# Kernel tuning notes

Measured on AMD Instinct MI355X. Metric: run time of the kernel, lower is better.

Reference implementation:

```python
import jax, jax.numpy as jnp
import numpy as np

N, E, D_IN, D_HID, D_OUT, G = 50000, 800000, 64, 64, 64, 64
BN_EPS = 1e-5


def gcn_conv(x, W, b, src, dst, n_nodes):
    """PyG GCNConv: add self-loops, sym-normalized sum aggregation, then bias.
    out_i = sum_{j->i} d_j^-1/2 d_i^-1/2 (x W)_j + d_i^-1 (x W)_i + b
    where d_i = 1 + in-degree(i) (self-loop included)."""
    h = x @ W  # [N, out]
    deg = jax.ops.segment_sum(jnp.ones((src.shape[0],), h.dtype), dst,
                              num_segments=n_nodes) + 1.0  # self-loop
    dinv = jax.lax.rsqrt(deg)  # deg >= 1 always
    coef = dinv[src] * dinv[dst]  # [E]
    msgs = h[src] * coef[:, None]  # [E, out] -- the big gather
    agg = jax.ops.segment_sum(msgs, dst, num_segments=n_nodes)
    agg = agg + h * (dinv * dinv)[:, None]  # self-loop messages
    return agg + b


def global_mean_pool(x, batch, n_graphs):
    sums = jax.ops.segment_sum(x, batch, num_segments=n_graphs)
    cnts = jax.ops.segment_sum(jnp.ones((x.shape[0],), x.dtype), batch,
                               num_segments=n_graphs)
    return sums / jnp.maximum(cnts, 1.0)[:, None]


def setup_inputs() -> dict:
    key = jax.random.key(0)
    ks = jax.random.split(key, 8)
    x = jax.random.normal(ks[0], (N, D_IN), dtype=jnp.float32)
    edge_index = jax.random.randint(ks[1], (2, E), 0, N, dtype=jnp.int32)
    batch = jnp.sort(jax.random.randint(ks[2], (N,), 0, G, dtype=jnp.int32))
    s1 = 1.0 / np.sqrt(D_IN)
    s2 = 1.0 / np.sqrt(D_HID)
    W1 = jax.random.uniform(ks[3], (D_IN, D_HID), jnp.float32, -s1, s1)
    b1 = jnp.zeros((D_HID,), jnp.float32)
    gamma = jnp.ones((D_HID,), jnp.float32)
    beta = jnp.zeros((D_HID,), jnp.float32)
    W2 = jax.random.uniform(ks[4], (D_HID, D_OUT), jnp.float32, -s2, s2)
    b2 = jnp.zeros((D_OUT,), jnp.float32)
    return {"x": x, "edge_index": edge_index, "batch": batch,
            "W1": W1, "b1": b1, "gamma": gamma, "beta": beta,
            "W2": W2, "b2": b2}


def reference(x, edge_index, batch, W1, b1, gamma, beta, W2, b2):
    src, dst = edge_index[0], edge_index[1]
    h = gcn_conv(x, W1, b1, src, dst, N)
    # BatchNorm1d with batch statistics (training-mode forward)
    mu = jnp.mean(h, axis=0)
    var = jnp.mean(jnp.square(h - mu), axis=0)
    h = (h - mu) * jax.lax.rsqrt(var + BN_EPS) * gamma + beta
    h = jax.nn.elu(h)
    # dropout is identity in eval / deterministic reference
    out = gcn_conv(h, W2, b2, src, dst, N)
    graph_rep = global_mean_pool(out, batch, G)
    return (out, graph_rep)
```

## Files before the change

kernel.cpp:

```cpp
#include <hip/hip_runtime.h>


constexpr int GGRAPHS = 64;
constexpr int EPB = 4096;
constexpr int CNTB = 128;

__global__ void fat_phist_cnt_mm64_kernel(
    const int* __restrict__ dst, const int* __restrict__ batch,
    int* __restrict__ hist, int* __restrict__ cnt,
    const float* __restrict__ X, const float* __restrict__ W,
    float* __restrict__ Y,
    int E, int n, int nblk, int nbuck) {
  __shared__ float Ws[64][64];
  __shared__ float xs[4][64];
  __shared__ int h[256];
  __shared__ int hb[GGRAPHS];
  int t = threadIdx.x;
  int bid = blockIdx.x;
  if (bid < nblk) {
    h[t] = 0;
    __syncthreads();
    int e0 = bid * EPB;
    int e1 = e0 + EPB < E ? e0 + EPB : E;
    for (int i = e0 + t; i < e1; i += 256) {
      int d = dst[i];
      if ((unsigned)d < (unsigned)n) atomicAdd(&h[d >> 8], 1);
    }
    __syncthreads();
    if (t < nbuck) hist[t * nblk + bid] = h[t];
  } else if (bid < nblk + CNTB) {
    int cb = bid - nblk;
    if (t < GGRAPHS) hb[t] = 0;
    __syncthreads();
    for (int i = cb * 256 + t; i < n; i += CNTB * 256) {
      int g = batch[i];
      if ((unsigned)g < (unsigned)GGRAPHS) atomicAdd(&hb[g], 1);
    }
    __syncthreads();
    if (t < GGRAPHS && hb[t] > 0) atomicAdd(&cnt[t], hb[t]);
  } else {
    int mb = bid - nblk - CNTB;
    for (int i = t; i < 64 * 64; i += 256) Ws[i >> 6][i & 63] = W[i];
    int rr = t >> 6, c = t & 63;
    int row = mb * 4 + rr;
    xs[rr][c] = (row < n) ? X[(size_t)row * 64 + c] : 0.0f;
    __syncthreads();
    float acc = 0.0f;
#pragma unroll
    for (int k = 0; k < 64; ++k) acc = fmaf(xs[rr][k], Ws[k][c], acc);
    if (row < n) Y[(size_t)row * 64 + c] = acc;
  }
}

__global__ void scan1_kernel(const int* __restrict__ in, int* __restrict__ out,
                             int* __restrict__ bsum, int n) {
  __shared__ int tmp[256];
  int t = threadIdx.x;
  int i = blockIdx.x * 256 + t;
  int v = (i < n) ? in[i] : 0;
  tmp[t] = v;
  __syncthreads();
#pragma unroll
  for (int off = 1; off < 256; off <<= 1) {
    int a = (t >= off) ? tmp[t - off] : 0;
    __syncthreads();
    tmp[t] += a;
    __syncthreads();
  }
  if (i < n) out[i] = tmp[t] - v;
  if (t == 255) bsum[blockIdx.x] = tmp[255];
}

__global__ void scan_add2_kernel(int* __restrict__ data, const int* __restrict__ bsum,
                                 int S, int nbt) {
  __shared__ int tmp[256];
  int t = threadIdx.x;
  int v = (t < nbt) ? bsum[t] : 0;
  tmp[t] = v;
  __syncthreads();
#pragma unroll
  for (int off = 1; off < 256; off <<= 1) {
    int a = (t >= off) ? tmp[t - off] : 0;
    __syncthreads();
    tmp[t] += a;
    __syncthreads();
  }
  int pre = (blockIdx.x == 0) ? 0 : tmp[blockIdx.x - 1];
  int i = blockIdx.x * 256 + t;
  if (i < S) data[i] += pre;
  if (i == 0) data[S] = tmp[nbt - 1];
}

__global__ void part_kernel(const int* __restrict__ srcp, const int* __restrict__ dstp,
                            const int* __restrict__ hist, int* __restrict__ part,
                            int E, int n, int nblk, int nbuck) {
  __shared__ int cur[256];
  int t = threadIdx.x;
  if (t < nbuck) cur[t] = hist[t * nblk + blockIdx.x];
  __syncthreads();
  int e0 = blockIdx.x * EPB;
  int e1 = e0 + EPB < E ? e0 + EPB : E;
  for (int i = e0 + t; i < e1; i += 256) {
    int d = dstp[i];
    if ((unsigned)d >= (unsigned)n) continue;
    int s = srcp[i];
    int pos = atomicAdd(&cur[d >> 8], 1);
    part[pos] = (s << 8) | (d & 255);
  }
}

__global__ void csr_kernel(const int* __restrict__ part, const int* __restrict__ hist,
                           int* __restrict__ rowptr, float* __restrict__ dinv,
                           int* __restrict__ col, int n, int nblk, int nbuck) {
  __shared__ int degL[256], scn[256], cur[256];
  int t = threadIdx.x;
  int b = blockIdx.x;
  degL[t] = 0;
  cur[t] = 0;
  __syncthreads();
  int base = hist[b * nblk];
  int end = hist[(b + 1) * nblk];
  for (int i = base + t; i < end; i += 256) atomicAdd(&degL[part[i] & 255], 1);
  __syncthreads();
  int dv = degL[t];
  scn[t] = dv;
  __syncthreads();
#pragma unroll
  for (int off = 1; off < 256; off <<= 1) {
    int a = (t >= off) ? scn[t - off] : 0;
    __syncthreads();
    scn[t] += a;
    __syncthreads();
  }
  int excl = scn[t] - dv;
  int node = (b << 8) + t;
  if (node < n) {
    rowptr[node] = base + excl;
    dinv[node] = rsqrtf((float)dv + 1.0f);
  }
  if (b == nbuck - 1 && t == 0) rowptr[n] = end;
  scn[t] = excl;
  __syncthreads();
  for (int i = base + t; i < end; i += 256) {
    int u = part[i];
    int d = u & 255;
    int k = atomicAdd(&cur[d], 1);
    col[base + scn[d] + k] = u >> 8;
  }
}

__global__ void bn_elu_mm64_kernel(const float* __restrict__ X, const float* __restrict__ W,
                                   const float* __restrict__ ss, float* __restrict__ Y, int n) {
  __shared__ float Ws[64][64];
  __shared__ float xs[4][64];
  int tid = threadIdx.x;
  for (int i = tid; i < 64 * 64; i += 256) Ws[i >> 6][i & 63] = W[i];
  int rr = tid >> 6, c = tid & 63;
  int row = blockIdx.x * 4 + rr;
  float v = 0.0f;
  if (row < n) {
    v = X[(size_t)row * 64 + c] * ss[c] + ss[64 + c];
    v = v > 0.0f ? v : expm1f(v);
  }
  xs[rr][c] = v;
  __syncthreads();
  float acc = 0.0f;
#pragma unroll
  for (int k = 0; k < 64; ++k) acc = fmaf(xs[rr][k], Ws[k][c], acc);
  if (row < n) Y[(size_t)row * 64 + c] = acc;
}

__device__ __forceinline__ float4 gcn_gather_core(
    const int* __restrict__ rowptr, const int* __restrict__ col,
    const float* __restrict__ dinv, const float4* __restrict__ H4,
    int row, int lane, int sub, int cg, bool valid) {
  float4 acc = make_float4(0.f, 0.f, 0.f, 0.f);
  int p0 = 0, p1 = 0;
  if (valid) { p0 = rowptr[row]; p1 = rowptr[row + 1]; }
  for (int base = p0; base < p1; base += 64) {
    int myp = base + lane;
    int j = (myp < p1) ? col[myp] : 0;
    float w = (myp < p1) ? dinv[j] : 0.0f;
    int m = p1 - base;
    m = m < 64 ? m : 64;
#pragma unroll 4
    for (int k = 0; k < m; k += 4) {
      int s = k + sub;
      int jj = __shfl(j, s);
      float ww = __shfl(w, s);
      float4 hv = H4[(size_t)jj * 16 + cg];
      acc.x = fmaf(hv.x, ww, acc.x);
      acc.y = fmaf(hv.y, ww, acc.y);
      acc.z = fmaf(hv.z, ww, acc.z);
      acc.w = fmaf(hv.w, ww, acc.w);
    }
  }
  acc.x += __shfl_xor(acc.x, 16);
  acc.y += __shfl_xor(acc.y, 16);
  acc.z += __shfl_xor(acc.z, 16);
  acc.w += __shfl_xor(acc.w, 16);
  acc.x += __shfl_xor(acc.x, 32);
  acc.y += __shfl_xor(acc.y, 32);
  acc.z += __shfl_xor(acc.z, 32);
  acc.w += __shfl_xor(acc.w, 32);
  return acc;
}

__global__ void gather_bn_kernel(const int* __restrict__ rowptr, const int* __restrict__ col,
                                 const float* __restrict__ dinv, const float* __restrict__ H,
                                 const float* __restrict__ b, float* __restrict__ OUT,
                                 float* __restrict__ bnsR, int n) {
  int wave = threadIdx.x >> 6;
  int lane = threadIdx.x & 63;
  int row = blockIdx.x * 4 + wave;
  bool valid = row < n;
  int sub = lane >> 4;
  int cg = lane & 15;
  const float4* __restrict__ H4 = (const float4*)H;
  float4 acc = gcn_gather_core(rowptr, col, dinv, H4, row, lane, sub, cg, valid);
  float4 o = make_float4(0.f, 0.f, 0.f, 0.f);
  if (valid) {
    float di = dinv[row];
    float d2 = di * di;
    float4 self = H4[(size_t)row * 16 + cg];
    float4 bb = ((const float4*)b)[cg];
    o.x = fmaf(acc.x, di, fmaf(self.x, d2, bb.x));
    o.y = fmaf(acc.y, di, fmaf(self.y, d2, bb.y));
    o.z = fmaf(acc.z, di, fmaf(self.z, d2, bb.z));
    o.w = fmaf(acc.w, di, fmaf(self.w, d2, bb.w));
    if (sub == 0) ((float4*)OUT)[(size_t)row * 16 + cg] = o;
  }
  __shared__ float sA[4][64], sB[4][64];
  if (sub == 0) {
    sA[wave][4 * cg + 0] = o.x;
    sA[wave][4 * cg + 1] = o.y;
    sA[wave][4 * cg + 2] = o.z;
    sA[wave][4 * cg + 3] = o.w;
    sB[wave][4 * cg + 0] = o.x * o.x;
    sB[wave][4 * cg + 1] = o.y * o.y;
    sB[wave][4 * cg + 2] = o.z * o.z;
    sB[wave][4 * cg + 3] = o.w * o.w;
  }
  __syncthreads();
  int t = threadIdx.x;
  if (t < 64) {
    float s = sA[0][t] + sA[1][t] + sA[2][t] + sA[3][t];
    float s2 = sB[0][t] + sB[1][t] + sB[2][t] + sB[3][t];
    float* d = bnsR + (size_t)(blockIdx.x & 255) * 128;
    atomicAdd(&d[t], s);
    atomicAdd(&d[64 + t], s2);
  }
}

__global__ void gather_pool_kernel(const int* __restrict__ rowptr, const int* __restrict__ col,
                                   const float* __restrict__ dinv, const float* __restrict__ H,
                                   const float* __restrict__ b, float* __restrict__ OUT,
                                   const int* __restrict__ batch, float* __restrict__ poolR,
                                   int n) {
  int wave = threadIdx.x >> 6;
  int lane = threadIdx.x & 63;
  int row = blockIdx.x * 4 + wave;
  bool valid = row < n;
  int sub = lane >> 4;
  int cg = lane & 15;
  const float4* __restrict__ H4 = (const float4*)H;
  float4 acc = gcn_gather_core(rowptr, col, dinv, H4, row, lane, sub, cg, valid);
  float4 o = make_float4(0.f, 0.f, 0.f, 0.f);
  __shared__ float sO[4][64];
  __shared__ int sG[4];
  if (valid) {
    float di = dinv[row];
    float d2 = di * di;
    float4 self = H4[(size_t)row * 16 + cg];
    float4 bb = ((const float4*)b)[cg];
    o.x = fmaf(acc.x, di, fmaf(self.x, d2, bb.x));
    o.y = fmaf(acc.y, di, fmaf(self.y, d2, bb.y));
    o.z = fmaf(acc.z, di, fmaf(self.z, d2, bb.z));
    o.w = fmaf(acc.w, di, fmaf(self.w, d2, bb.w));
    if (sub == 0) ((float4*)OUT)[(size_t)row * 16 + cg] = o;
  }
  if (lane == 0) {
    int g = valid ? batch[row] : -1;
    sG[wave] = ((unsigned)g < (unsigned)GGRAPHS) ? g : -1;
  }
  if (sub == 0) {
    sO[wave][4 * cg + 0] = o.x;
    sO[wave][4 * cg + 1] = o.y;
    sO[wave][4 * cg + 2] = o.z;
    sO[wave][4 * cg + 3] = o.w;
  }
  __syncthreads();
  int t = threadIdx.x;
  if (t < 64) {
    float* base = poolR + (size_t)(blockIdx.x & 15) * 4096;
    int g0 = sG[0];
    float s0 = 0.0f;
#pragma unroll
    for (int w = 0; w < 4; ++w) {
      int gw = sG[w];
      if (gw < 0) continue;
      if (gw == g0) s0 += sO[w][t];
      else atomicAdd(&base[gw * 64 + t], sO[w][t]);
    }
    if (g0 >= 0) atomicAdd(&base[g0 * 64 + t], s0);
  }
}

__global__ void bn_final_kernel(const float* __restrict__ bnsR, const float* __restrict__ gamma,
                                const float* __restrict__ beta, float* __restrict__ ss, int n) {
  __shared__ float red[128];
  int t = threadIdx.x;
  float s = 0.0f;
  for (int r = 0; r < 256; ++r) s += bnsR[r * 128 + t];
  red[t] = s;
  __syncthreads();
  if (t < 64) {
    float inv_n = 1.0f / (float)n;
    float mu = red[t] * inv_n;
    float var = red[64 + t] * inv_n - mu * mu;
    var = fmaxf(var, 0.0f);
    float sc = gamma[t] * rsqrtf(var + 1e-5f);
    ss[t] = sc;
    ss[64 + t] = beta[t] - mu * sc;
  }
}

__global__ void pool_final_kernel(const float* __restrict__ poolR, const int* __restrict__ cnt,
                                  float* __restrict__ out) {
  int idx = blockIdx.x * 256 + threadIdx.x;
  float s = 0.0f;
  for (int r = 0; r < 16; ++r) s += poolR[r * 4096 + idx];
  int g = idx >> 6;
  float c = (float)cnt[g];
  out[idx] = s / fmaxf(c, 1.0f);
}

extern "C" void kernel_launch(void* const* d_in, const int* in_sizes, int n_in,
                              void* d_out, int out_size, void* d_ws, size_t ws_size,
                              hipStream_t stream) {
  const float* x = (const float*)d_in[0];
  const int* ei = (const int*)d_in[1];
  const int* batch = (const int*)d_in[2];
  const float* W1 = (const float*)d_in[3];
  const float* b1 = (const float*)d_in[4];
  const float* gamma = (const float*)d_in[5];
  const float* beta = (const float*)d_in[6];
  const float* W2 = (const float*)d_in[7];
  const float* b2 = (const float*)d_in[8];

  const int n = in_sizes[0] / 64;
  const int E = in_sizes[1] / 2;
  const int* srcp = ei;
  const int* dstp = ei + E;

  int nblkP = (E + EPB - 1) / EPB;
  int nbuck = (n + 255) >> 8;
  int S = nbuck * nblkP;
  int nbt = (S + 255) / 256;
  int gridRows = (n + 3) / 4;

  float* ws = (float*)d_ws;
  size_t nf = (size_t)n * 64;
  float* bufA = ws;
  float* bufB = ws + nf;
  float* dinv = ws + 2 * nf;
  float* ss = dinv + n;
  int* rowptr = (int*)(ss + 128);
  int* col = rowptr + n + 1;
  int* part = col + E;
  int* hist = part + E;
  int* bsum = hist + S + 1;
  float* bnsR = (float*)(bsum + 256);
  float* poolR = bnsR + 256 * 128;
  int* cnti = (int*)(poolR + 16 * 4096);

  float* out = (float*)d_out;

  size_t zbytes = (size_t)((char*)(cnti + 64) - (char*)bnsR);
  hipMemsetAsync(bnsR, 0, zbytes, stream);

  int blk = 256;
  int fatGrid = nblkP + CNTB + gridRows;

  fat_phist_cnt_mm64_kernel<<<fatGrid, blk, 0, stream>>>(
      dstp, batch, hist, cnti, x, W1, bufA, E, n, nblkP, nbuck);
  scan1_kernel<<<nbt, blk, 0, stream>>>(hist, hist, bsum, S);
  scan_add2_kernel<<<nbt, blk, 0, stream>>>(hist, bsum, S, nbt);
  part_kernel<<<nblkP, blk, 0, stream>>>(srcp, dstp, hist, part, E, n, nblkP, nbuck);
  csr_kernel<<<nbuck, blk, 0, stream>>>(part, hist, rowptr, dinv, col, n, nblkP, nbuck);

  gather_bn_kernel<<<gridRows, blk, 0, stream>>>(rowptr, col, dinv, bufA, b1, bufB, bnsR, n);
  bn_final_kernel<<<1, 128, 0, stream>>>(bnsR, gamma, beta, ss, n);
  bn_elu_mm64_kernel<<<gridRows, blk, 0, stream>>>(bufB, W2, ss, bufA, n);
  gather_pool_kernel<<<gridRows, blk, 0, stream>>>(rowptr, col, dinv, bufA, b2, out, batch,
                                                   poolR, n);
  pool_final_kernel<<<16, blk, 0, stream>>>(poolR, cnti, out + nf);
}
```

Baseline: 258.3 us.

## Cut kernel launches by fusing memset, scan fixup, and finalizers into neighbors

Replaces the memset with zeroing blocks inside the first fused kernel. The second-level scan fixup is dropped, so part_kernel and csr_kernel each redo the small block-sum scan locally. The BN-statistics and pool finalizers are folded into the last block of the gather kernels using a last-block ticket counter. Graph counts become per-block partials instead of atomics. This removes four launches and their serialization gaps, at the cost of extra fences, a redundant scan in every block, and a serialized tail in the last block.

```diff
diff --git a/kernel.cpp b/kernel.cpp
--- a/kernel.cpp
+++ b/kernel.cpp
@@ -4,10 +4,11 @@
 constexpr int GGRAPHS = 64;
 constexpr int EPB = 4096;
 constexpr int CNTB = 128;
-
-__global__ void fat_phist_cnt_mm64_kernel(
+constexpr int ZBLK = 32;
+
+__global__ void fat_phist_cnt_zero_mm64_kernel(
     const int* __restrict__ dst, const int* __restrict__ batch,
-    int* __restrict__ hist, int* __restrict__ cnt,
+    int* __restrict__ hist, int* __restrict__ cntR, float* __restrict__ zbase,
     const float* __restrict__ X, const float* __restrict__ W,
     float* __restrict__ Y,
     int E, int n, int nblk, int nbuck) {
@@ -37,9 +38,15 @@
       if ((unsigned)g < (unsigned)GGRAPHS) atomicAdd(&hb[g], 1);
     }
     __syncthreads();
-    if (t < GGRAPHS && hb[t] > 0) atomicAdd(&cnt[t], hb[t]);
+    if (t < GGRAPHS) cntR[cb * 64 + t] = hb[t];
+  } else if (bid < nblk + CNTB + ZBLK) {
+    int zb = bid - nblk - CNTB;
+    float4 z4 = make_float4(0.f, 0.f, 0.f, 0.f);
+    int tot4 = (256 * 128 + 16 * 4096 + 4) >> 2;
+    float4* d4 = (float4*)zbase;
+    for (int i = zb * 256 + t; i < tot4; i += ZBLK * 256) d4[i] = z4;
   } else {
-    int mb = bid - nblk - CNTB;
+    int mb = bid - nblk - CNTB - ZBLK;
     for (int i = t; i < 64 * 64; i += 256) Ws[i >> 6][i & 63] = W[i];
     int rr = t >> 6, c = t & 63;
     int row = mb * 4 + rr;
@@ -71,9 +78,12 @@
   if (t == 255) bsum[blockIdx.x] = tmp[255];
 }
 
-__global__ void scan_add2_kernel(int* __restrict__ data, const int* __restrict__ bsum,
-                                 int S, int nbt) {
+__global__ void part_kernel(const int* __restrict__ srcp, const int* __restrict__ dstp,
+                            const int* __restrict__ hist, const int* __restrict__ bsum,
+                            int* __restrict__ part, int E, int n, int nblk, int nbuck,
+                            int nbt) {
   __shared__ int tmp[256];
+  __shared__ int cur[256];
   int t = threadIdx.x;
   int v = (t < nbt) ? bsum[t] : 0;
   tmp[t] = v;
@@ -85,18 +95,12 @@
     tmp[t] += a;
     __syncthreads();
   }
-  int pre = (blockIdx.x == 0) ? 0 : tmp[blockIdx.x - 1];
-  int i = blockIdx.x * 256 + t;
-  if (i < S) data[i] += pre;
-  if (i == 0) data[S] = tmp[nbt - 1];
-}
-
-__global__ void part_kernel(const int* __restrict__ srcp, const int* __restrict__ dstp,
-                            const int* __restrict__ hist, int* __restrict__ part,
-                            int E, int n, int nblk, int nbuck) {
-  __shared__ int cur[256];
-  int t = threadIdx.x;
-  if (t < nbuck) cur[t] = hist[t * nblk + blockIdx.x];
+  if (t < nbuck) {
+    int idx = t * nblk + blockIdx.x;
+    int tile = idx >> 8;
+    int pre = (tile == 0) ? 0 : tmp[tile - 1];
+    cur[t] = hist[idx] + pre;
+  }
   __syncthreads();
   int e0 = blockIdx.x * EPB;
   int e1 = e0 + EPB < E ? e0 + EPB : E;
@@ -110,16 +114,31 @@
 }
 
 __global__ void csr_kernel(const int* __restrict__ part, const int* __restrict__ hist,
+                           const int* __restrict__ bsum,
                            int* __restrict__ rowptr, float* __restrict__ dinv,
-                           int* __restrict__ col, int n, int nblk, int nbuck) {
+                           int* __restrict__ col, int n, int nblk, int nbuck,
+                           int nbt, int S) {
+  __shared__ int tmpb[256];
   __shared__ int degL[256], scn[256], cur[256];
   int t = threadIdx.x;
   int b = blockIdx.x;
+  int v = (t < nbt) ? bsum[t] : 0;
+  tmpb[t] = v;
   degL[t] = 0;
   cur[t] = 0;
   __syncthreads();
-  int base = hist[b * nblk];
-  int end = hist[(b + 1) * nblk];
+#pragma unroll
+  for (int off = 1; off < 256; off <<= 1) {
+    int a = (t >= off) ? tmpb[t - off] : 0;
+    __syncthreads();
+    tmpb[t] += a;
+    __syncthreads();
+  }
+  int bidx = b * nblk;
+  int eidx = bidx + nblk;
+  int base = hist[bidx] + ((bidx >> 8) ? tmpb[(bidx >> 8) - 1] : 0);
+  int total = tmpb[nbt - 1];
+  int end = (eidx < S) ? hist[eidx] + ((eidx >> 8) ? tmpb[(eidx >> 8) - 1] : 0) : total;
   for (int i = base + t; i < end; i += 256) atomicAdd(&degL[part[i] & 255], 1);
   __syncthreads();
   int dv = degL[t];
@@ -209,7 +228,11 @@
 __global__ void gather_bn_kernel(const int* __restrict__ rowptr, const int* __restrict__ col,
                                  const float* __restrict__ dinv, const float* __restrict__ H,
                                  const float* __restrict__ b, float* __restrict__ OUT,
-                                 float* __restrict__ bnsR, int n) {
+                                 float* __restrict__ bnsR, int* __restrict__ tick,
+                                 const float* __restrict__ gamma, const float* __restrict__ beta,
+                                 float* __restrict__ ss, int n) {
+  __shared__ float sA[4][64], sB[4][64];
+  __shared__ int isLast;
   int wave = threadIdx.x >> 6;
   int lane = threadIdx.x & 63;
   int row = blockIdx.x * 4 + wave;
@@ -230,7 +253,6 @@
     o.w = fmaf(acc.w, di, fmaf(self.w, d2, bb.w));
     if (sub == 0) ((float4*)OUT)[(size_t)row * 16 + cg] = o;
   }
-  __shared__ float sA[4][64], sB[4][64];
   if (sub == 0) {
     sA[wave][4 * cg + 0] = o.x;
     sA[wave][4 * cg + 1] = o.y;
@@ -250,13 +272,45 @@
     atomicAdd(&d[t], s);
     atomicAdd(&d[64 + t], s2);
   }
+  __syncthreads();
+  if (t == 0) {
+    __threadfence();
+    int old = atomicAdd(tick, 1);
+    isLast = (old == (int)gridDim.x - 1) ? 1 : 0;
+  }
+  __syncthreads();
+  if (isLast) {
+    __threadfence();
+    float s = 0.0f;
+    if (t < 128) {
+      for (int r = 0; r < 256; ++r)
+        s += __hip_atomic_load(&bnsR[r * 128 + t], __ATOMIC_RELAXED, __HIP_MEMORY_SCOPE_AGENT);
+    }
+    float* red = (float*)sA;
+    if (t < 128) red[t] = s;
+    __syncthreads();
+    if (t < 64) {
+      float inv_n = 1.0f / (float)n;
+      float mu = red[t] * inv_n;
+      float var = red[64 + t] * inv_n - mu * mu;
+      var = fmaxf(var, 0.0f);
+      float sc = gamma[t] * rsqrtf(var + 1e-5f);
+      ss[t] = sc;
+      ss[64 + t] = beta[t] - mu * sc;
+    }
+  }
 }
 
 __global__ void gather_pool_kernel(const int* __restrict__ rowptr, const int* __restrict__ col,
                                    const float* __restrict__ dinv, const float* __restrict__ H,
                                    const float* __restrict__ b, float* __restrict__ OUT,
                                    const int* __restrict__ batch, float* __restrict__ poolR,
-                                   int n) {
+                                   int* __restrict__ tick, const int* __restrict__ cntR,
+                                   float* __restrict__ outG, int n) {
+  __shared__ float sO[4][64];
+  __shared__ int sG[4];
+  __shared__ int isLast;
+  __shared__ float cgc[64];
   int wave = threadIdx.x >> 6;
   int lane = threadIdx.x & 63;
   int row = blockIdx.x * 4 + wave;
@@ -266,8 +320,6 @@
   const float4* __restrict__ H4 = (const float4*)H;
   float4 acc = gcn_gather_core(rowptr, col, dinv, H4, row, lane, sub, cg, valid);
   float4 o = make_float4(0.f, 0.f, 0.f, 0.f);
-  __shared__ float sO[4][64];
-  __shared__ int sG[4];
   if (valid) {
     float di = dinv[row];
     float d2 = di * di;
@@ -304,35 +356,29 @@
     }
     if (g0 >= 0) atomicAdd(&base[g0 * 64 + t], s0);
   }
-}
-
-__global__ void bn_final_kernel(const float* __restrict__ bnsR, const float* __restrict__ gamma,
-                                const float* __restrict__ beta, float* __restrict__ ss, int n) {
-  __shared__ float red[128];
-  int t = threadIdx.x;
-  float s = 0.0f;
-  for (int r = 0; r < 256; ++r) s += bnsR[r * 128 + t];
-  red[t] = s;
-  __syncthreads();
-  if (t < 64) {
-    float inv_n = 1.0f / (float)n;
-    float mu = red[t] * inv_n;
-    float var = red[64 + t] * inv_n - mu * mu;
-    var = fmaxf(var, 0.0f);
-    float sc = gamma[t] * rsqrtf(var + 1e-5f);
-    ss[t] = sc;
-    ss[64 + t] = beta[t] - mu * sc;
-  }
-}
-
-__global__ void pool_final_kernel(const float* __restrict__ poolR, const int* __restrict__ cnt,
-                                  float* __restrict__ out) {
-  int idx = blockIdx.x * 256 + threadIdx.x;
-  float s = 0.0f;
-  for (int r = 0; r < 16; ++r) s += poolR[r * 4096 + idx];
-  int g = idx >> 6;
-  float c = (float)cnt[g];
-  out[idx] = s / fmaxf(c, 1.0f);
+  __syncthreads();
+  if (t == 0) {
+    __threadfence();
+    int old = atomicAdd(tick, 1);
+    isLast = (old == (int)gridDim.x - 1) ? 1 : 0;
+  }
+  __syncthreads();
+  if (isLast) {
+    __threadfence();
+    if (t < 64) {
+      int c = 0;
+      for (int cb = 0; cb < CNTB; ++cb) c += cntR[cb * 64 + t];
+      cgc[t] = (float)c;
+    }
+    __syncthreads();
+    for (int idx = t; idx < GGRAPHS * 64; idx += 256) {
+      float s = 0.0f;
+      for (int r = 0; r < 16; ++r)
+        s += __hip_atomic_load(&poolR[r * 4096 + idx], __ATOMIC_RELAXED,
+                               __HIP_MEMORY_SCOPE_AGENT);
+      outG[idx] = s / fmaxf(cgc[idx >> 6], 1.0f);
+    }
+  }
 }
 
 extern "C" void kernel_launch(void* const* d_in, const int* in_sizes, int n_in,
@@ -370,29 +416,27 @@
   int* part = col + E;
   int* hist = part + E;
   int* bsum = hist + S + 1;
-  float* bnsR = (float*)(bsum + 256);
+  float* bnsR = (float*)(((uintptr_t)(bsum + 256) + 15) & ~(uintptr_t)15);
   float* poolR = bnsR + 256 * 128;
-  int* cnti = (int*)(poolR + 16 * 4096);
+  int* tick = (int*)(poolR + 16 * 4096);
+  int* cntR = tick + 4;
 
   float* out = (float*)d_out;
 
-  size_t zbytes = (size_t)((char*)(cnti + 64) - (char*)bnsR);
-  hipMemsetAsync(bnsR, 0, zbytes, stream);
-
   int blk = 256;
-  int fatGrid = nblkP + CNTB + gridRows;
-
-  fat_phist_cnt_mm64_kernel<<<fatGrid, blk, 0, stream>>>(
-      dstp, batch, hist, cnti, x, W1, bufA, E, n, nblkP, nbuck);
+  int fatGrid = nblkP + CNTB + ZBLK + gridRows;
+
+  fat_phist_cnt_zero_mm64_kernel<<<fatGrid, blk, 0, stream>>>(
+      dstp, batch, hist, cntR, bnsR, x, W1, bufA, E, n, nblkP, nbuck);
   scan1_kernel<<<nbt, blk, 0, stream>>>(hist, hist, bsum, S);
-  scan_add2_kernel<<<nbt, blk, 0, stream>>>(hist, bsum, S, nbt);
-  part_kernel<<<nblkP, blk, 0, stream>>>(srcp, dstp, hist, part, E, n, nblkP, nbuck);
-  csr_kernel<<<nbuck, blk, 0, stream>>>(part, hist, rowptr, dinv, col, n, nblkP, nbuck);
-
-  gather_bn_kernel<<<gridRows, blk, 0, stream>>>(rowptr, col, dinv, bufA, b1, bufB, bnsR, n);
-  bn_final_kernel<<<1, 128, 0, stream>>>(bnsR, gamma, beta, ss, n);
+  part_kernel<<<nblkP, blk, 0, stream>>>(srcp, dstp, hist, bsum, part, E, n, nblkP,
+                                         nbuck, nbt);
+  csr_kernel<<<nbuck, blk, 0, stream>>>(part, hist, bsum, rowptr, dinv, col, n, nblkP,
+                                        nbuck, nbt, S);
+
+  gather_bn_kernel<<<gridRows, blk, 0, stream>>>(rowptr, col, dinv, bufA, b1, bufB, bnsR,
+                                                 &tick[0], gamma, beta, ss, n);
   bn_elu_mm64_kernel<<<gridRows, blk, 0, stream>>>(bufB, W2, ss, bufA, n);
   gather_pool_kernel<<<gridRows, blk, 0, stream>>>(rowptr, col, dinv, bufA, b2, out, batch,
-                                                   poolR, n);
-  pool_final_kernel<<<16, blk, 0, stream>>>(poolR, cnti, out + nf);
-}
+                                                   poolR, &tick[1], cntR, out + nf, n);
+}
```

After: 863.3 us. 234% more time.
